# Optimization experiments

Hardware: AMD Instinct MI355X
Metric: run time of the kernel (lower is better)

## Reference

```python
import jax, jax.numpy as jnp
import numpy as np

LMDA = 1.0
SMOOTH = 1e-05

# 13 directional offsets (dz, dy, dx) matching the original slice pairs 1..13
OFFSETS = [
    (1, 0, 0), (0, 1, 0), (0, 0, 1),
    (1, 1, 0), (1, -1, 0),
    (0, 1, 1), (0, 1, -1),
    (1, 0, -1), (1, 0, 1),
    (1, -1, -1), (1, 1, -1),
    (-1, -1, -1), (-1, 1, -1),
]


def _shifted_diff(x, off):
    """x[..., pos-shift] - x[..., neg-shift] for offset off over last 3 dims."""
    sl_pos = tuple(slice(1, None) if o == 1 else (slice(None, -1) if o == -1 else slice(None)) for o in off)
    sl_neg = tuple(slice(None, -1) if o == 1 else (slice(1, None) if o == -1 else slice(None)) for o in off)
    return x[(Ellipsis,) + sl_pos] - x[(Ellipsis,) + sl_neg]


def setup_inputs() -> dict:
    key = jax.random.key(0)
    k1, k2 = jax.random.split(key)
    shape = (4, 1, 128, 192, 192)
    eps = 1e-6
    inp = jax.random.uniform(k1, shape, dtype=jnp.float32, minval=eps, maxval=1.0 - eps)
    tgt = jax.random.uniform(k2, shape, dtype=jnp.float32, minval=0.0, maxval=1.0)
    return {"input": inp, "target": tgt}


def reference(input, target):
    # region term: BCE with mean reduction
    bce = -jnp.mean(target * jnp.log(input) + (1.0 - target) * jnp.log(1.0 - input))

    # boundary term: 13 directional diff-product ratios
    acc = jnp.float32(0.0)
    for off in OFFSETS:
        di = _shifted_diff(input, off)
        dt = _shifted_diff(target, off)
        acc = acc + jnp.sum(di * dt) / (jnp.sum(dt * dt) + SMOOTH)
    boundary = 1.0 - acc / 13.0

    return LMDA * bce + boundary
```

## Files before the change

### kernel.cpp

```cpp
#include <hip/hip_runtime.h>
#include <math.h>

#define DX 192
#define DY 192
#define DZ 128
#define DB 4
#define DXY (DX*DY)
#define NTOT ((long)DB*DZ*DY*DX)
#define NV ((unsigned)(NTOT/4))
#define XV (DX/4)
#define NBLK 1536


typedef float v2f __attribute__((ext_vector_type(2)));

struct __attribute__((packed, aligned(4))) f4u { float x, y, z, w; };

__device__ __forceinline__ float4 ld4 (const float* p){ return *(const float4*)p; }
__device__ __forceinline__ float4 ld4u(const float* p){
    f4u t = *(const f4u*)p;
    float4 r; r.x=t.x; r.y=t.y; r.z=t.z; r.w=t.w; return r;
}
__device__ __forceinline__ v2f lo(float4 a){ v2f r = {a.x, a.y}; return r; }
__device__ __forceinline__ v2f hi(float4 a){ v2f r = {a.z, a.w}; return r; }
__device__ __forceinline__ v2f spl(float s){ v2f r = {s, s}; return r; }

__device__ __forceinline__ void core(
    v2f c0,v2f c1,v2f c2,v2f c3,v2f c4,v2f c5,v2f c6,v2f c7,
    v2f d0,v2f d1,v2f d2,v2f d3,v2f d4,v2f d5,v2f d6,v2f d7,
    v2f mx, v2f mzy, v2f myx, v2f mzx, v2f mzyx, v2f (&A)[27])
{
    v2f di, dt, dtm;
    di=c4-c0; dt=d4-d0;              A[0] +=di*dt;  A[13]+=dt*dt;
    di=c2-c0; dt=d2-d0;              A[1] +=di*dt;  A[14]+=dt*dt;
    di=c1-c0; dt=d1-d0; dtm=mx*dt;   A[2] +=di*dtm; A[15]+=dt*dtm;
    di=c6-c0; dt=d6-d0; dtm=mzy*dt;  A[3] +=di*dtm; A[16]+=dt*dtm;
    di=c4-c2; dt=d4-d2; dtm=mzy*dt;  A[4] +=di*dtm; A[17]+=dt*dtm;
    di=c3-c0; dt=d3-d0; dtm=myx*dt;  A[5] +=di*dtm; A[18]+=dt*dtm;
    di=c2-c1; dt=d2-d1; dtm=myx*dt;  A[6] +=di*dtm; A[19]+=dt*dtm;
    di=c4-c1; dt=d4-d1; dtm=mzx*dt;  A[7] +=di*dtm; A[20]+=dt*dtm;
    di=c5-c0; dt=d5-d0; dtm=mzx*dt;  A[8] +=di*dtm; A[21]+=dt*dtm;
    di=c4-c3; dt=d4-d3; dtm=mzyx*dt; A[9] +=di*dtm; A[22]+=dt*dtm;
    di=c6-c1; dt=d6-d1; dtm=mzyx*dt; A[10]+=di*dtm; A[23]+=dt*dtm;
    di=c7-c0; dt=d7-d0; dtm=mzyx*dt; A[11]+=di*dtm; A[24]+=dt*dtm;
    di=c5-c2; dt=d5-d2; dtm=mzyx*dt; A[12]+=di*dtm; A[25]+=dt*dtm;
}

__global__ __launch_bounds__(256) void gc3d_main(const float* __restrict__ inp,
                                                 const float* __restrict__ tgt,
                                                 double* __restrict__ acc)
{
    v2f A[27];
    #pragma unroll
    for (int k = 0; k < 27; ++k) A[k] = spl(0.f);

    unsigned tid = blockIdx.x * 256 + threadIdx.x;
    const unsigned stride = NBLK * 256;

    #pragma unroll 1
    for (unsigned v = tid; v < NV; v += stride) {
        unsigned xv4 = v % XV;
        unsigned rem = v / XV;
        unsigned y   = rem % DY;
        unsigned z   = (rem / DY) & (DZ - 1);

        size_t base = (size_t)v * 4;
        const float* ip = inp + base;
        const float* tp = tgt + base;
        int   oy  = (y < DY-1) ? DX  : 0;
        int   oz  = (z < DZ-1) ? DXY : 0;
        float fy  = (y < DY-1) ? 1.f : 0.f;
        float fz  = (z < DZ-1) ? 1.f : 0.f;
        float fx3 = (xv4 < XV-1) ? 1.f : 0.f;
        int   xo  = (base + (size_t)oz + (size_t)oy + 8 <= (size_t)NTOT) ? 1 : 0;
        float fzy = fz * fy;

        float4 i00=ld4(ip),        i00x=ld4u(ip+xo);
        float4 i01=ld4(ip+oy),     i01x=ld4u(ip+oy+xo);
        float4 i10=ld4(ip+oz),     i10x=ld4u(ip+oz+xo);
        float4 i11=ld4(ip+oz+oy),  i11x=ld4u(ip+oz+oy+xo);
        float4 t00=ld4(tp),        t00x=ld4u(tp+xo);
        float4 t01=ld4(tp+oy),     t01x=ld4u(tp+oy+xo);
        float4 t10=ld4(tp+oz),     t10x=ld4u(tp+oz+xo);
        float4 t11=ld4(tp+oz+oy),  t11x=ld4u(tp+oz+oy+xo);

        {
            v2f one = {1.f, 1.f};
            core(lo(i00),lo(i00x),lo(i01),lo(i01x),lo(i10),lo(i10x),lo(i11),lo(i11x),
                 lo(t00),lo(t00x),lo(t01),lo(t01x),lo(t10),lo(t10x),lo(t11),lo(t11x),
                 one, spl(fzy), spl(fy), spl(fz), spl(fzy), A);
            v2f p = lo(i00), q = lo(t00);
            v2f l0 = { __logf(p.x),       __logf(p.y)       };
            v2f l1 = { __logf(1.f - p.x), __logf(1.f - p.y) };
            A[26] += l1 + q * (l0 - l1);
        }
        {
            v2f fxv = {1.f, fx3};
            core(hi(i00),hi(i00x),hi(i01),hi(i01x),hi(i10),hi(i10x),hi(i11),hi(i11x),
                 hi(t00),hi(t00x),hi(t01),hi(t01x),hi(t10),hi(t10x),hi(t11),hi(t11x),
                 fxv, spl(fzy), fxv*fy, fxv*fz, fxv*fzy, A);
            v2f p = hi(i00), q = hi(t00);
            v2f l0 = { __logf(p.x),       __logf(p.y)       };
            v2f l1 = { __logf(1.f - p.x), __logf(1.f - p.y) };
            A[26] += l1 + q * (l0 - l1);
        }
    }

    float vals[27];
    #pragma unroll
    for (int k = 0; k < 27; ++k) vals[k] = A[k].x + A[k].y;
    #pragma unroll
    for (int k = 0; k < 27; ++k) {
        #pragma unroll
        for (int o = 32; o > 0; o >>= 1) vals[k] += __shfl_down(vals[k], o, 64);
    }

    __shared__ float red[4][27];
    int lane = threadIdx.x & 63;
    int wave = threadIdx.x >> 6;
    if (lane == 0) {
        #pragma unroll
        for (int k = 0; k < 27; ++k) red[wave][k] = vals[k];
    }
    __syncthreads();
    if (threadIdx.x < 27) {
        float t = red[0][threadIdx.x] + red[1][threadIdx.x]
                + red[2][threadIdx.x] + red[3][threadIdx.x];
        atomicAdd(&acc[threadIdx.x], (double)t);
    }
}

__global__ void gc3d_final(const double* __restrict__ acc, float* __restrict__ out) {
    if (threadIdx.x == 0 && blockIdx.x == 0) {
        double s = 0.0;
        #pragma unroll
        for (int k = 0; k < 13; ++k) s += acc[k] / (acc[13 + k] + 1e-5);
        double bce = -acc[26] / (double)NTOT;
        out[0] = (float)(bce + 1.0 - s / 13.0);
    }
}

extern "C" void kernel_launch(void* const* d_in, const int* in_sizes, int n_in,
                              void* d_out, int out_size, void* d_ws, size_t ws_size,
                              hipStream_t stream) {
    const float* inp = (const float*)d_in[0];
    const float* tgt = (const float*)d_in[1];
    double* acc = (double*)d_ws;

    hipMemsetAsync(d_ws, 0, 27 * sizeof(double), stream);
    gc3d_main<<<NBLK, 256, 0, stream>>>(inp, tgt, acc);
    gc3d_final<<<1, 64, 0, stream>>>(acc, (float*)d_out);
}
```

Before: 226.2 us.

## Replace unaligned neighbor loads with scalar edge loads and add interior fast path

The kernel drops the second, unaligned float4 load per neighbor row. It now reads one extra scalar per row to get the x+1 neighbor, which cuts load traffic and the cost of unaligned accesses. Math moves from packed 2-wide vectors to scalar, run over 4 elements per group. A wave-uniform interior branch skips the boundary mask multiplies. The grid-stride loop is unrolled by two for more memory-level parallelism, with an occupancy hint in launch_bounds. Losing packed FP32 math and adding registers could offset the gains.

```diff
diff --git a/kernel.cpp b/kernel.cpp
--- a/kernel.cpp
+++ b/kernel.cpp
@@ -12,115 +12,130 @@
 #define NBLK 1536
 
 
-typedef float v2f __attribute__((ext_vector_type(2)));
+struct Grp {
+    float4 i00, i01, i10, i11, t00, t01, t10, t11;
+    float  i00e, i01e, i10e, i11e, t00e, t01e, t10e, t11e;
+};
 
-struct __attribute__((packed, aligned(4))) f4u { float x, y, z, w; };
-
-__device__ __forceinline__ float4 ld4 (const float* p){ return *(const float4*)p; }
-__device__ __forceinline__ float4 ld4u(const float* p){
-    f4u t = *(const f4u*)p;
-    float4 r; r.x=t.x; r.y=t.y; r.z=t.z; r.w=t.w; return r;
-}
-__device__ __forceinline__ v2f lo(float4 a){ v2f r = {a.x, a.y}; return r; }
-__device__ __forceinline__ v2f hi(float4 a){ v2f r = {a.z, a.w}; return r; }
-__device__ __forceinline__ v2f spl(float s){ v2f r = {s, s}; return r; }
-
-__device__ __forceinline__ void core(
-    v2f c0,v2f c1,v2f c2,v2f c3,v2f c4,v2f c5,v2f c6,v2f c7,
-    v2f d0,v2f d1,v2f d2,v2f d3,v2f d4,v2f d5,v2f d6,v2f d7,
-    v2f mx, v2f mzy, v2f myx, v2f mzx, v2f mzyx, v2f (&A)[27])
+__device__ __forceinline__ void load_grp(Grp& g, const float* __restrict__ ip,
+                                         const float* __restrict__ tp,
+                                         int oy, int oz, int xe)
 {
-    v2f di, dt, dtm;
-    di=c4-c0; dt=d4-d0;              A[0] +=di*dt;  A[13]+=dt*dt;
-    di=c2-c0; dt=d2-d0;              A[1] +=di*dt;  A[14]+=dt*dt;
-    di=c1-c0; dt=d1-d0; dtm=mx*dt;   A[2] +=di*dtm; A[15]+=dt*dtm;
-    di=c6-c0; dt=d6-d0; dtm=mzy*dt;  A[3] +=di*dtm; A[16]+=dt*dtm;
-    di=c4-c2; dt=d4-d2; dtm=mzy*dt;  A[4] +=di*dtm; A[17]+=dt*dtm;
-    di=c3-c0; dt=d3-d0; dtm=myx*dt;  A[5] +=di*dtm; A[18]+=dt*dtm;
-    di=c2-c1; dt=d2-d1; dtm=myx*dt;  A[6] +=di*dtm; A[19]+=dt*dtm;
-    di=c4-c1; dt=d4-d1; dtm=mzx*dt;  A[7] +=di*dtm; A[20]+=dt*dtm;
-    di=c5-c0; dt=d5-d0; dtm=mzx*dt;  A[8] +=di*dtm; A[21]+=dt*dtm;
-    di=c4-c3; dt=d4-d3; dtm=mzyx*dt; A[9] +=di*dtm; A[22]+=dt*dtm;
-    di=c6-c1; dt=d6-d1; dtm=mzyx*dt; A[10]+=di*dtm; A[23]+=dt*dtm;
-    di=c7-c0; dt=d7-d0; dtm=mzyx*dt; A[11]+=di*dtm; A[24]+=dt*dtm;
-    di=c5-c2; dt=d5-d2; dtm=mzyx*dt; A[12]+=di*dtm; A[25]+=dt*dtm;
+    g.i00 = *(const float4*)(ip);            g.i00e = ip[xe];
+    g.i01 = *(const float4*)(ip + oy);       g.i01e = ip[oy + xe];
+    g.i10 = *(const float4*)(ip + oz);       g.i10e = ip[oz + xe];
+    g.i11 = *(const float4*)(ip + oz + oy);  g.i11e = ip[oz + oy + xe];
+    g.t00 = *(const float4*)(tp);            g.t00e = tp[xe];
+    g.t01 = *(const float4*)(tp + oy);       g.t01e = tp[oy + xe];
+    g.t10 = *(const float4*)(tp + oz);       g.t10e = tp[oz + xe];
+    g.t11 = *(const float4*)(tp + oz + oy);  g.t11e = tp[oz + oy + xe];
 }
 
-__global__ __launch_bounds__(256) void gc3d_main(const float* __restrict__ inp,
-                                                 const float* __restrict__ tgt,
-                                                 double* __restrict__ acc)
+template<bool INTERIOR>
+__device__ __forceinline__ void compute_grp(const Grp& g, float fz, float fy,
+                                            float fx3, float (&A)[27])
 {
-    v2f A[27];
+    const float I0[5] = {g.i00.x, g.i00.y, g.i00.z, g.i00.w, g.i00e};
+    const float I1[5] = {g.i01.x, g.i01.y, g.i01.z, g.i01.w, g.i01e};
+    const float J0[5] = {g.i10.x, g.i10.y, g.i10.z, g.i10.w, g.i10e};
+    const float J1[5] = {g.i11.x, g.i11.y, g.i11.z, g.i11.w, g.i11e};
+    const float T0[5] = {g.t00.x, g.t00.y, g.t00.z, g.t00.w, g.t00e};
+    const float T1[5] = {g.t01.x, g.t01.y, g.t01.z, g.t01.w, g.t01e};
+    const float U0[5] = {g.t10.x, g.t10.y, g.t10.z, g.t10.w, g.t10e};
+    const float U1[5] = {g.t11.x, g.t11.y, g.t11.z, g.t11.w, g.t11e};
+    const float fzy = fz * fy;
+
     #pragma unroll
-    for (int k = 0; k < 27; ++k) A[k] = spl(0.f);
+    for (int e = 0; e < 4; ++e) {
+        const float fx = (e < 3) ? 1.0f : fx3;
+        float mzy, myx, mzx, mzyx;
+        if (INTERIOR) { mzy = 1.f; myx = 1.f; mzx = 1.f; mzyx = 1.f; }
+        else { mzy = fzy; myx = fy*fx; mzx = fz*fx; mzyx = fzy*fx; }
+        const float c0=I0[e], c1=I0[e+1], c2=I1[e], c3=I1[e+1];
+        const float c4=J0[e], c5=J0[e+1], c6=J1[e], c7=J1[e+1];
+        const float d0=T0[e], d1=T0[e+1], d2=T1[e], d3=T1[e+1];
+        const float d4=U0[e], d5=U0[e+1], d6=U1[e], d7=U1[e+1];
+        float di, dt, dtm;
+        di=c4-c0; dt=d4-d0;              A[0] +=di*dt;  A[13]+=dt*dt;
+        di=c2-c0; dt=d2-d0;              A[1] +=di*dt;  A[14]+=dt*dt;
+        di=c1-c0; dt=d1-d0;              A[2] +=di*dt;  A[15]+=dt*dt;
+        di=c6-c0; dt=d6-d0; dtm=mzy*dt;  A[3] +=di*dtm; A[16]+=dt*dtm;
+        di=c4-c2; dt=d4-d2; dtm=mzy*dt;  A[4] +=di*dtm; A[17]+=dt*dtm;
+        di=c3-c0; dt=d3-d0; dtm=myx*dt;  A[5] +=di*dtm; A[18]+=dt*dtm;
+        di=c2-c1; dt=d2-d1; dtm=myx*dt;  A[6] +=di*dtm; A[19]+=dt*dtm;
+        di=c4-c1; dt=d4-d1; dtm=mzx*dt;  A[7] +=di*dtm; A[20]+=dt*dtm;
+        di=c5-c0; dt=d5-d0; dtm=mzx*dt;  A[8] +=di*dtm; A[21]+=dt*dtm;
+        di=c4-c3; dt=d4-d3; dtm=mzyx*dt; A[9] +=di*dtm; A[22]+=dt*dtm;
+        di=c6-c1; dt=d6-d1; dtm=mzyx*dt; A[10]+=di*dtm; A[23]+=dt*dtm;
+        di=c7-c0; dt=d7-d0; dtm=mzyx*dt; A[11]+=di*dtm; A[24]+=dt*dtm;
+        di=c5-c2; dt=d5-d2; dtm=mzyx*dt; A[12]+=di*dtm; A[25]+=dt*dtm;
+        float l0 = __logf(c0), l1 = __logf(1.0f - c0);
+        A[26] += l1 + d0 * (l0 - l1);
+    }
+}
+
+__device__ __forceinline__ void prep(unsigned v, const float* __restrict__ inp,
+                                     const float* __restrict__ tgt,
+                                     const float*& ip, const float*& tp,
+                                     int& oy, int& oz, int& xe,
+                                     float& fz, float& fy, float& fx3, int& intr)
+{
+    unsigned xv4 = v % XV;
+    unsigned rem = v / XV;
+    unsigned y   = rem % DY;
+    unsigned z   = (rem / DY) & (DZ - 1);
+    ip = inp + (size_t)v * 4;
+    tp = tgt + (size_t)v * 4;
+    bool by = (y   < DY-1), bz = (z < DZ-1), bx = (xv4 < XV-1);
+    oy  = by ? DX  : 0;
+    oz  = bz ? DXY : 0;
+    xe  = bx ? 4 : 3;
+    fy  = by ? 1.f : 0.f;
+    fz  = bz ? 1.f : 0.f;
+    fx3 = bx ? 1.f : 0.f;
+    intr = (by && bz && bx) ? 1 : 0;
+}
+
+__global__ __launch_bounds__(256, 4) void gc3d_main(const float* __restrict__ inp,
+                                                    const float* __restrict__ tgt,
+                                                    double* __restrict__ acc)
+{
+    float A[27];
+    #pragma unroll
+    for (int k = 0; k < 27; ++k) A[k] = 0.f;
 
     unsigned tid = blockIdx.x * 256 + threadIdx.x;
     const unsigned stride = NBLK * 256;
 
     #pragma unroll 1
-    for (unsigned v = tid; v < NV; v += stride) {
-        unsigned xv4 = v % XV;
-        unsigned rem = v / XV;
-        unsigned y   = rem % DY;
-        unsigned z   = (rem / DY) & (DZ - 1);
+    for (unsigned v = tid; v < NV; v += 2 * stride) {
+        const float *ip1, *tp1, *ip2, *tp2;
+        int oy1, oz1, xe1, i1, oy2, oz2, xe2, i2;
+        float fz1, fy1, fx1, fz2, fy2, fx2;
+        prep(v,          inp, tgt, ip1, tp1, oy1, oz1, xe1, fz1, fy1, fx1, i1);
+        prep(v + stride, inp, tgt, ip2, tp2, oy2, oz2, xe2, fz2, fy2, fx2, i2);
 
-        size_t base = (size_t)v * 4;
-        const float* ip = inp + base;
-        const float* tp = tgt + base;
-        int   oy  = (y < DY-1) ? DX  : 0;
-        int   oz  = (z < DZ-1) ? DXY : 0;
-        float fy  = (y < DY-1) ? 1.f : 0.f;
-        float fz  = (z < DZ-1) ? 1.f : 0.f;
-        float fx3 = (xv4 < XV-1) ? 1.f : 0.f;
-        int   xo  = (base + (size_t)oz + (size_t)oy + 8 <= (size_t)NTOT) ? 1 : 0;
-        float fzy = fz * fy;
+        Grp g1, g2;
+        load_grp(g1, ip1, tp1, oy1, oz1, xe1);
+        load_grp(g2, ip2, tp2, oy2, oz2, xe2);
 
-        float4 i00=ld4(ip),        i00x=ld4u(ip+xo);
-        float4 i01=ld4(ip+oy),     i01x=ld4u(ip+oy+xo);
-        float4 i10=ld4(ip+oz),     i10x=ld4u(ip+oz+xo);
-        float4 i11=ld4(ip+oz+oy),  i11x=ld4u(ip+oz+oy+xo);
-        float4 t00=ld4(tp),        t00x=ld4u(tp+xo);
-        float4 t01=ld4(tp+oy),     t01x=ld4u(tp+oy+xo);
-        float4 t10=ld4(tp+oz),     t10x=ld4u(tp+oz+xo);
-        float4 t11=ld4(tp+oz+oy),  t11x=ld4u(tp+oz+oy+xo);
-
-        {
-            v2f one = {1.f, 1.f};
-            core(lo(i00),lo(i00x),lo(i01),lo(i01x),lo(i10),lo(i10x),lo(i11),lo(i11x),
-                 lo(t00),lo(t00x),lo(t01),lo(t01x),lo(t10),lo(t10x),lo(t11),lo(t11x),
-                 one, spl(fzy), spl(fy), spl(fz), spl(fzy), A);
-            v2f p = lo(i00), q = lo(t00);
-            v2f l0 = { __logf(p.x),       __logf(p.y)       };
-            v2f l1 = { __logf(1.f - p.x), __logf(1.f - p.y) };
-            A[26] += l1 + q * (l0 - l1);
-        }
-        {
-            v2f fxv = {1.f, fx3};
-            core(hi(i00),hi(i00x),hi(i01),hi(i01x),hi(i10),hi(i10x),hi(i11),hi(i11x),
-                 hi(t00),hi(t00x),hi(t01),hi(t01x),hi(t10),hi(t10x),hi(t11),hi(t11x),
-                 fxv, spl(fzy), fxv*fy, fxv*fz, fxv*fzy, A);
-            v2f p = hi(i00), q = hi(t00);
-            v2f l0 = { __logf(p.x),       __logf(p.y)       };
-            v2f l1 = { __logf(1.f - p.x), __logf(1.f - p.y) };
-            A[26] += l1 + q * (l0 - l1);
-        }
+        if (__all(i1)) compute_grp<true >(g1, fz1, fy1, fx1, A);
+        else           compute_grp<false>(g1, fz1, fy1, fx1, A);
+        if (__all(i2)) compute_grp<true >(g2, fz2, fy2, fx2, A);
+        else           compute_grp<false>(g2, fz2, fy2, fx2, A);
     }
 
-    float vals[27];
-    #pragma unroll
-    for (int k = 0; k < 27; ++k) vals[k] = A[k].x + A[k].y;
     #pragma unroll
     for (int k = 0; k < 27; ++k) {
         #pragma unroll
-        for (int o = 32; o > 0; o >>= 1) vals[k] += __shfl_down(vals[k], o, 64);
+        for (int o = 32; o > 0; o >>= 1) A[k] += __shfl_down(A[k], o, 64);
     }
-
     __shared__ float red[4][27];
     int lane = threadIdx.x & 63;
     int wave = threadIdx.x >> 6;
     if (lane == 0) {
         #pragma unroll
-        for (int k = 0; k < 27; ++k) red[wave][k] = vals[k];
+        for (int k = 0; k < 27; ++k) red[wave][k] = A[k];
     }
     __syncthreads();
     if (threadIdx.x < 27) {
```

After: 631.6 us. +179.3%, slower.
